# Kernel optimization log

Hardware: AMD Instinct MI355X
Metric: run time of the kernel (lower is better)

The kernel has to match this reference:

```python
import jax, jax.numpy as jnp
import numpy as np

D_SUMMARY = 128
N_LAYERS = 24
N_HEADS = 16
D_HEAD = 64
HIDDEN = 512
ACTIVE_MIN = 12
ROT = 16
THETA = 10000.0
B, P = 16, 128
L_ACT = N_LAYERS - ACTIVE_MIN
OUT_DIM = N_HEADS * 2 * D_HEAD


def setup_inputs() -> dict:
    key = jax.random.key(0)
    k1, k2, k3, k4, k5, k6 = jax.random.split(key, 6)
    summary_stack = jax.random.normal(k1, (B, P, D_SUMMARY), jnp.float32)
    positions = jnp.sort(jax.random.randint(k2, (P,), 0, 8192))
    s1 = 1.0 / np.sqrt(D_SUMMARY)
    s2 = 1.0 / np.sqrt(HIDDEN)
    W1 = jax.random.uniform(k3, (L_ACT, D_SUMMARY, HIDDEN), jnp.float32, -s1, s1)
    b1 = jax.random.uniform(k4, (L_ACT, HIDDEN), jnp.float32, -s1, s1)
    W2 = jax.random.uniform(k5, (L_ACT, HIDDEN, OUT_DIM), jnp.float32, -s2, s2)
    b2 = jax.random.uniform(k6, (L_ACT, OUT_DIM), jnp.float32, -s2, s2)
    return {"summary_stack": summary_stack, "positions": positions,
            "W1": W1, "b1": b1, "W2": W2, "b2": b2}


def reference(summary_stack, positions, W1, b1, W2, b2):
    # Batched 2-layer MLP across all active layers (grouped GEMM)
    h = jax.nn.relu(jnp.einsum('bps,lsh->lbph', summary_stack, W1) + b1[:, None, None, :])
    kv = jnp.einsum('lbph,lho->lbpo', h, W2) + b2[:, None, None, :]
    kv = kv.reshape(L_ACT, B, P, N_HEADS, 2, D_HEAD)
    k = jnp.transpose(kv[..., 0, :], (0, 1, 3, 2, 4))  # (L,B,H,P,D)
    v = jnp.transpose(kv[..., 1, :], (0, 1, 3, 2, 4))
    # RoPE on first ROT dims of K
    inv_freq = 1.0 / (THETA ** (jnp.arange(0, ROT, 2, dtype=jnp.float32) / ROT))
    freqs = positions.astype(jnp.float32)[:, None] * inv_freq[None, :]  # (P, ROT//2)
    emb = jnp.concatenate([freqs, freqs], axis=-1)  # (P, ROT)
    cos, sin = jnp.cos(emb), jnp.sin(emb)
    k_rot, k_pass = k[..., :ROT], k[..., ROT:]
    rot_half = jnp.concatenate([-k_rot[..., ROT // 2:], k_rot[..., :ROT // 2]], axis=-1)
    k_emb = k_rot * cos + rot_half * sin
    k = jnp.concatenate([k_emb, k_pass], axis=-1)
    # Inactive layers get zero K/V
    zeros = jnp.zeros((ACTIVE_MIN, B, N_HEADS, P, D_HEAD), k.dtype)
    k_all = jnp.concatenate([zeros, k], axis=0)
    v_all = jnp.concatenate([zeros, v], axis=0)
    return jnp.stack([k_all, v_all], axis=1)  # (n_layers, 2, B, H, P, D)
```

## Files before the change

### kernel.cpp

```cpp
#include <hip/hip_runtime.h>
#include <hip/hip_bf16.h>

#define L_ACT   12
#define BDIM    16
#define PDIM    128
#define DSUM    128
#define HID     512
#define ODIM    2048
#define NHEAD   16
#define DHEAD   64
#define MROWS   2048

typedef short s16x4  __attribute__((ext_vector_type(4)));
typedef short short8 __attribute__((ext_vector_type(8)));
typedef float f32x4  __attribute__((ext_vector_type(4)));

__device__ __forceinline__ void gload_lds16(const __hip_bfloat16* g, __hip_bfloat16* l) {
  __builtin_amdgcn_global_load_lds(
      (const __attribute__((address_space(1))) unsigned int*)g,
      (__attribute__((address_space(3))) unsigned int*)l, 16, 0, 0);
}

__device__ __forceinline__ short f2bf(float x) {
  __hip_bfloat16 h = __float2bfloat16(x);
  return *reinterpret_cast<short*>(&h);
}

__global__ __launch_bounds__(256) void zerofill_kernel(f32x4* __restrict__ p, int n16) {
  int stride = gridDim.x * 256;
  for (int i = blockIdx.x * 256 + threadIdx.x; i < n16; i += stride)
    p[i] = {0.f, 0.f, 0.f, 0.f};
}

__global__ __launch_bounds__(256) void gemm1_128(
    const float* __restrict__ summary,
    const float* __restrict__ W1,
    const int*   __restrict__ positions,
    const float* __restrict__ bias,
    __hip_bfloat16* __restrict__ Hall,
    const float* __restrict__ W2,
    __hip_bfloat16* __restrict__ W2T,
    float* __restrict__ cs,
    f32x4* __restrict__ zeroBase, int doZero) {
  const int KTOT = DSUM, NTOT = HID;
  __shared__ __hip_bfloat16 shbuf[24576];
  __hip_bfloat16* ldsB2 = shbuf;
  __hip_bfloat16* ldsA  = shbuf + 16384;
  const int l    = blockIdx.z;
  const int n0   = blockIdx.x * 128;
  const int m0   = blockIdx.y * 128;
  const int tid  = threadIdx.x;
  const int wid  = tid >> 6;
  const int lane = tid & 63;
  const int wr = wid >> 1, wc = wid & 1;
  const int bid = blockIdx.x + 4 * blockIdx.y + 64 * blockIdx.z;

  if (bid == 0) {
#pragma unroll
    for (int q = 0; q < 4; ++q) {
      int i = q * 256 + tid;
      int p = i >> 3, f = i & 7;
      double inv = pow(10000.0, -(double)f / 8.0);
      double ang = (double)positions[p] * inv;
      cs[i]        = (float)cos(ang);
      cs[1024 + i] = (float)sin(ang);
    }
  }

  {
    const float* Wp = W1 + (size_t)l * DSUM * HID + n0;
#pragma unroll
    for (int q = 0; q < 16; ++q) {
      int g  = q * 256 + tid;
      int j4 = g >> 7;
      int r  = g & 127;
      s16x4 w;
#pragma unroll
      for (int jj = 0; jj < 4; ++jj)
        w[jj] = f2bf(Wp[(size_t)(j4 * 4 + jj) * HID + r]);
      int chunk = (j4 >> 1) ^ (r & 7);
      *(s16x4*)((char*)ldsB2 + r * 256 + chunk * 16 + (j4 & 1) * 8) = w;
    }
  }

  f32x4 acc[4][4];
#pragma unroll
  for (int m = 0; m < 4; ++m)
#pragma unroll
    for (int n = 0; n < 4; ++n)
      acc[m][n] = {0.f, 0.f, 0.f, 0.f};

  const int kq = lane >> 4;

  for (int kt = 0; kt < KTOT / 64; ++kt) {
    __syncthreads();
#pragma unroll
    for (int j = 0; j < 8; ++j) {
      int s = j * 256 + tid;
      int r = s >> 4, g = s & 15;
      f32x4 v = *(const f32x4*)(summary + (size_t)(m0 + r) * DSUM + kt * 64 + g * 4);
      s16x4 w;
      w[0] = f2bf(v[0]); w[1] = f2bf(v[1]); w[2] = f2bf(v[2]); w[3] = f2bf(v[3]);
      int ch = g >> 1;
      *(s16x4*)((char*)ldsA + r * 128 + ((ch ^ (r & 7)) << 4) + (g & 1) * 8) = w;
    }
    __syncthreads();
#pragma unroll
    for (int kk = 0; kk < 2; ++kk) {
      short8 af[4], bfr[4];
#pragma unroll
      for (int m = 0; m < 4; ++m) {
        int row = wr * 64 + m * 16 + (lane & 15);
        int off = (kk * 64 + kq * 16) ^ ((row & 7) << 4);
        af[m] = *(const short8*)((const char*)ldsA + row * 128 + off);
      }
#pragma unroll
      for (int n = 0; n < 4; ++n) {
        int row = wc * 64 + n * 16 + (lane & 15);
        int chunk = (kt * 8 + kk * 4 + kq) ^ (row & 7);
        bfr[n] = *(const short8*)((const char*)ldsB2 + row * 256 + chunk * 16);
      }
#pragma unroll
      for (int m = 0; m < 4; ++m)
#pragma unroll
        for (int n = 0; n < 4; ++n)
          acc[m][n] = __builtin_amdgcn_mfma_f32_16x16x32_bf16(af[m], bfr[n], acc[m][n], 0, 0, 0);
    }
  }

  __syncthreads();
#pragma unroll
  for (int n = 0; n < 4; ++n) {
    int col = wc * 64 + n * 16 + (lane & 15);
    float bb = bias[l * NTOT + n0 + col];
#pragma unroll
    for (int m = 0; m < 4; ++m) {
      int rowb = wr * 64 + m * 16 + ((lane >> 4) << 2);
#pragma unroll
      for (int j = 0; j < 4; ++j) {
        float v = acc[m][n][j] + bb;
        v = v > 0.f ? v : 0.f;
        shbuf[(rowb + j) * 136 + col] = __float2bfloat16(v);
      }
    }
  }
  __syncthreads();
  {
    __hip_bfloat16* H = Hall + (size_t)l * MROWS * HID;
#pragma unroll
    for (int i = 0; i < 8; ++i) {
      int idx = i * 256 + tid;
      int row = idx >> 4, seg = idx & 15;
      short8 v = *(const short8*)(shbuf + row * 136 + seg * 8);
      *(short8*)(H + (size_t)(m0 + row) * HID + n0 + seg * 8) = v;
    }
  }
  __syncthreads();

  {
    float* tb0 = (float*)shbuf;
    float* tb1 = (float*)shbuf + 1056;
    const int tx = tid & 31, ty = tid >> 5;
    const int tbase = bid * 16;
    const f32x4 z = {0.f, 0.f, 0.f, 0.f};
    f32x4* zp = zeroBase + (size_t)bid * 8192;
    float rvA0, rvA1, rvA2, rvA3, rvB0, rvB1, rvB2, rvB3;

#define W2_LOAD(P, tt_) do {                                                \
      int t_ = tbase + (tt_);                                               \
      int lz_ = t_ >> 10, rem_ = t_ & 1023;                                 \
      int j0_ = (rem_ >> 6) * 32, o0_ = (rem_ & 63) * 32;                   \
      const float* ip_ = W2 + (size_t)lz_ * HID * ODIM                      \
                       + (size_t)(j0_ + ty) * ODIM + o0_ + tx;              \
      P##0 = ip_[0];                                                        \
      P##1 = ip_[(size_t)8 * ODIM];                                         \
      P##2 = ip_[(size_t)16 * ODIM];                                        \
      P##3 = ip_[(size_t)24 * ODIM];                                        \
    } while (0)

#define W2_WRITE(buf, P) do {                                               \
      (buf)[(ty +  0) * 33 + tx] = P##0;                                    \
      (buf)[(ty +  8) * 33 + tx] = P##1;                                    \
      (buf)[(ty + 16) * 33 + tx] = P##2;                                    \
      (buf)[(ty + 24) * 33 + tx] = P##3;                                    \
    } while (0)

#define W2_STORE(buf, tt_) do {                                             \
      int t_ = tbase + (tt_);                                               \
      int lz_ = t_ >> 10, rem_ = t_ & 1023;                                 \
      int j0_ = (rem_ >> 6) * 32, o0_ = (rem_ & 63) * 32;                   \
      __hip_bfloat16* op_ = W2T + (size_t)lz_ * HID * ODIM;                 \
      _Pragma("unroll")                                                     \
      for (int r_ = 0; r_ < 4; ++r_)                                        \
        op_[(size_t)(o0_ + ty + 8 * r_) * HID + j0_ + tx] =                 \
            __float2bfloat16((buf)[tx * 33 + ty + 8 * r_]);                 \
    } while (0)

#define ZCHUNK(tt_) do { if (doZero && (tt_) < 8) {                         \
      _Pragma("unroll")                                                     \
      for (int q_ = 0; q_ < 4; ++q_)                                        \
        __builtin_nontemporal_store(z, zp + ((tt_) * 4 + q_) * 256 + tid);  \
    } } while (0)

    W2_LOAD(rvA, 0);
    W2_LOAD(rvB, 1);
    W2_WRITE(tb0, rvA);
    __syncthreads();
#pragma unroll 1
    for (int tt = 0; tt < 16; tt += 2) {
      if (tt + 2 < 16) W2_LOAD(rvA, tt + 2);
      W2_STORE(tb0, tt);
      W2_WRITE(tb1, rvB);
      ZCHUNK(tt);
      __syncthreads();
      if (tt + 3 < 16) W2_LOAD(rvB, tt + 3);
      W2_STORE(tb1, tt + 1);
      if (tt + 2 < 16) W2_WRITE(tb0, rvA);
      ZCHUNK(tt + 1);
      __syncthreads();
    }
#undef W2_LOAD
#undef W2_WRITE
#undef W2_STORE
#undef ZCHUNK
  }
}

__global__ __launch_bounds__(256, 2) void gemm2_pipe(
    const __hip_bfloat16* __restrict__ Aall,
    const __hip_bfloat16* __restrict__ Ball,
    const float* __restrict__ bias,
    const float* __restrict__ cs,
    float* __restrict__ O,
    f32x4* __restrict__ zeroBase, int doZero) {
  __shared__ __hip_bfloat16 lds[3 * 12288];
  const int orig = blockIdx.x + 16 * blockIdx.y + 128 * blockIdx.z;
  const int nw   = (orig & 7) * 192 + (orig >> 3);
  const int bx   = nw & 15;
  const int by   = (nw >> 4) & 7;
  const int l    = nw >> 7;
  const int n0  = bx * 128;
  const int m0  = by * 256;
  const int tid = threadIdx.x;
  const int wid = tid >> 6, lane = tid & 63;
  const int wm  = wid >> 1, wn = wid & 1;
  const __hip_bfloat16* A  = Aall + (size_t)l * MROWS * HID;
  const __hip_bfloat16* Bt = Ball + (size_t)l * ODIM * HID;
  f32x4* zq = zeroBase + (size_t)nw * 4096;
  const f32x4 zv = {0.f, 0.f, 0.f, 0.f};

  f32x4 acc[8][4];
#pragma unroll
  for (int m = 0; m < 8; ++m)
#pragma unroll
    for (int n = 0; n < 4; ++n)
      acc[m][n] = {0.f, 0.f, 0.f, 0.f};

  int ra[4], ca[4], rb[2], cb[2];
#pragma unroll
  for (int j = 0; j < 4; ++j) {
    int cx = j * 256 + tid;
    ra[j] = cx >> 2; ca[j] = (cx & 3) ^ ((ra[j] >> 1) & 3);
  }
#pragma unroll
  for (int j = 0; j < 2; ++j) {
    int cx = j * 256 + tid;
    rb[j] = cx >> 2; cb[j] = (cx & 3) ^ ((rb[j] >> 1) & 3);
  }

#define STAGE_A(slot, kt) do {                                                      \
    _Pragma("unroll")                                                               \
    for (int j_ = 0; j_ < 4; ++j_)                                                  \
      gload_lds16(A + (size_t)(m0 + ra[j_]) * HID + (kt) * 32 + ca[j_] * 8,         \
                  lds + (slot) * 12288 + j_ * 2048 + wid * 512);                    \
  } while (0)
#define STAGE_B(slot, kt) do {                                                      \
    _Pragma("unroll")                                                               \
    for (int j_ = 0; j_ < 2; ++j_)                                                  \
      gload_lds16(Bt + (size_t)(n0 + rb[j_]) * HID + (kt) * 32 + cb[j_] * 8,        \
                  lds + (slot) * 12288 + 8192 + j_ * 2048 + wid * 512);             \
  } while (0)

  const int kq   = lane >> 4;
  const int rl15 = lane & 15;

#define LD_FRAG(dst, base, rr) do {                                                 \
    int r_ = (rr);                                                                  \
    int off_ = r_ * 64 + ((kq ^ ((r_ >> 1) & 3)) << 4);                             \
    dst = *(const short8*)((const char*)(base) + off_);                             \
  } while (0)

  STAGE_A(0, 0); STAGE_B(0, 0);
  STAGE_A(1, 1); STAGE_B(1, 1);
  asm volatile("s_waitcnt vmcnt(6)" ::: "memory");
  __builtin_amdgcn_s_barrier();

  const int NT = HID / 32;
  for (int t = 0; t < NT; ++t) {
    const int cur = t % 3;
    const __hip_bfloat16* sa = lds + cur * 12288;
    const __hip_bfloat16* sb = sa + 8192;
    short8 af[4], bfr[4];

    if (doZero)
      __builtin_nontemporal_store(zv, zq + t * 256 + tid);

#pragma unroll
    for (int n = 0; n < 4; ++n) LD_FRAG(bfr[n], sb, wn * 64 + n * 16 + rl15);
#pragma unroll
    for (int mi = 0; mi < 4; ++mi) LD_FRAG(af[mi], sa, wm * 128 + mi * 16 + rl15);
    if (t + 2 < NT) STAGE_A((t + 2) % 3, t + 2);
    __builtin_amdgcn_s_barrier();
    __builtin_amdgcn_s_setprio(1);
#pragma unroll
    for (int mi = 0; mi < 4; ++mi)
#pragma unroll
      for (int n = 0; n < 4; ++n)
        acc[mi][n] = __builtin_amdgcn_mfma_f32_16x16x32_bf16(af[mi], bfr[n], acc[mi][n], 0, 0, 0);
    __builtin_amdgcn_s_setprio(0);
    __builtin_amdgcn_s_barrier();

#pragma unroll
    for (int mi = 0; mi < 4; ++mi) LD_FRAG(af[mi], sa, wm * 128 + 64 + mi * 16 + rl15);
    if (t + 2 < NT) STAGE_B((t + 2) % 3, t + 2);
    __builtin_amdgcn_s_barrier();
    __builtin_amdgcn_s_setprio(1);
#pragma unroll
    for (int mi = 0; mi < 4; ++mi)
#pragma unroll
      for (int n = 0; n < 4; ++n)
        acc[4 + mi][n] = __builtin_amdgcn_mfma_f32_16x16x32_bf16(af[mi], bfr[n], acc[4 + mi][n], 0, 0, 0);
    __builtin_amdgcn_s_setprio(0);
    if (t < NT - 2)       asm volatile("s_waitcnt vmcnt(6)" ::: "memory");
    else if (t == NT - 2) asm volatile("s_waitcnt vmcnt(0)" ::: "memory");
    __builtin_amdgcn_s_barrier();
  }
#undef STAGE_A
#undef STAGE_B
#undef LD_FRAG

  __syncthreads();
  const int head = bx;
  const int tkv  = wn;
  const int bidx = by * 2 + wm;
  float* slab = O + ((((size_t)(l + L_ACT) * 2 + tkv) * BDIM + bidx) * NHEAD + head) * (PDIM * DHEAD);
  const bool ropeWave = (tkv == 0);

  float bb[4];
#pragma unroll
  for (int n = 0; n < 4; ++n) bb[n] = bias[l * ODIM + n0 + wn * 64 + n * 16 + rl15];

  float* Tw = (float*)lds + wid * 2080;

#pragma unroll
  for (int c = 0; c < 4; ++c) {
#pragma unroll
    for (int mh = 0; mh < 2; ++mh) {
      int mf = c * 2 + mh;
      int pl = mh * 16 + (lane >> 4) * 4;
#pragma unroll
      for (int n = 0; n < 4; ++n) {
#pragma unroll
        for (int j = 0; j < 4; ++j) {
          float v = acc[mf][n][j] + bb[n];
          if (ropeWave && n == 0) {
            float partner = __shfl_xor(v, 8);
            int p = c * 32 + pl + j;
            float cv = cs[p * 8 + (lane & 7)];
            float sv = cs[1024 + p * 8 + (lane & 7)];
            v = v * cv + (((lane & 15) < 8) ? -partner : partner) * sv;
          }
          Tw[(pl + j) * 65 + n * 16 + rl15] = v;
        }
      }
    }
#pragma unroll
    for (int it = 0; it < 8; ++it) {
      int pl = it * 4 + (lane >> 4);
      f32x4 vv = *(const f32x4*)(Tw + pl * 65 + rl15 * 4);
      __builtin_nontemporal_store(vv, (f32x4*)(slab + (size_t)(c * 32 + pl) * DHEAD + rl15 * 4));
    }
  }
}

extern "C" void kernel_launch(void* const* d_in, const int* in_sizes, int n_in,
                              void* d_out, int out_size, void* d_ws, size_t ws_size,
                              hipStream_t stream) {
  const float* summary   = (const float*)d_in[0];
  const int*   positions = (const int*)d_in[1];
  const float* W1 = (const float*)d_in[2];
  const float* b1 = (const float*)d_in[3];
  const float* W2 = (const float*)d_in[4];
  const float* b2 = (const float*)d_in[5];
  float* out = (float*)d_out;

  const size_t SCRATCH_BYTES = 25165824ULL + 25165824ULL + 8192ULL;
  const bool useWs = (ws_size >= SCRATCH_BYTES);
  char* sc = useWs ? (char*)d_ws : (char*)d_out;
  __hip_bfloat16* h_bf = (__hip_bfloat16*)sc;
  __hip_bfloat16* W2T  = (__hip_bfloat16*)(sc + 25165824);
  float*          cs   = (float*)(sc + 50331648);

  gemm1_128<<<dim3(HID / 128, MROWS / 128, L_ACT), 256, 0, stream>>>(
      summary, W1, positions, b1, h_bf, W2, W2T, cs,
      (f32x4*)((char*)d_out + 100663296), useWs ? 1 : 0);
  gemm2_pipe<<<dim3(ODIM / 128, MROWS / 256, L_ACT), 256, 0, stream>>>(
      h_bf, W2T, b2, cs, out, (f32x4*)d_out, useWs ? 1 : 0);

  if (!useWs)
    zerofill_kernel<<<2048, 256, 0, stream>>>((f32x4*)d_out, 12582912);
}
```

Measured before the change: 124.4 us.

## Overlap W2 prefetch and zero-fill stores with GEMM1 using LDS-only barriers

Issues the first W2 tile loads before the GEMM1 main loop and spreads the zero-fill stores for inactive layers across the GEMM1 k-loop and epilogue, so global memory traffic overlaps with MFMA work. It also swaps __syncthreads for a barrier that waits only on LDS counters (lgkmcnt), so in-flight global loads and stores do not stall each barrier. This keeps the prefetched registers live across the GEMM, which raises register pressure. It also relies on global stores never needing ordering at these barriers.

```diff
diff --git a/kernel.cpp b/kernel.cpp
--- a/kernel.cpp
+++ b/kernel.cpp
@@ -25,6 +25,11 @@
   __hip_bfloat16 h = __float2bfloat16(x);
   return *reinterpret_cast<short*>(&h);
 }
+
+#define LBAR() do {                                                   \
+    asm volatile("s_waitcnt lgkmcnt(0)" ::: "memory");                \
+    __builtin_amdgcn_s_barrier();                                     \
+  } while (0)
 
 __global__ __launch_bounds__(256) void zerofill_kernel(f32x4* __restrict__ p, int n16) {
   int stride = gridDim.x * 256;
@@ -55,6 +60,9 @@
   const int wr = wid >> 1, wc = wid & 1;
   const int bid = blockIdx.x + 4 * blockIdx.y + 64 * blockIdx.z;
 
+  const f32x4 z = {0.f, 0.f, 0.f, 0.f};
+  f32x4* zp = zeroBase + (size_t)bid * 8192;
+
   if (bid == 0) {
 #pragma unroll
     for (int q = 0; q < 4; ++q) {
@@ -67,104 +75,9 @@
     }
   }
 
-  {
-    const float* Wp = W1 + (size_t)l * DSUM * HID + n0;
-#pragma unroll
-    for (int q = 0; q < 16; ++q) {
-      int g  = q * 256 + tid;
-      int j4 = g >> 7;
-      int r  = g & 127;
-      s16x4 w;
-#pragma unroll
-      for (int jj = 0; jj < 4; ++jj)
-        w[jj] = f2bf(Wp[(size_t)(j4 * 4 + jj) * HID + r]);
-      int chunk = (j4 >> 1) ^ (r & 7);
-      *(s16x4*)((char*)ldsB2 + r * 256 + chunk * 16 + (j4 & 1) * 8) = w;
-    }
-  }
-
-  f32x4 acc[4][4];
-#pragma unroll
-  for (int m = 0; m < 4; ++m)
-#pragma unroll
-    for (int n = 0; n < 4; ++n)
-      acc[m][n] = {0.f, 0.f, 0.f, 0.f};
-
-  const int kq = lane >> 4;
-
-  for (int kt = 0; kt < KTOT / 64; ++kt) {
-    __syncthreads();
-#pragma unroll
-    for (int j = 0; j < 8; ++j) {
-      int s = j * 256 + tid;
-      int r = s >> 4, g = s & 15;
-      f32x4 v = *(const f32x4*)(summary + (size_t)(m0 + r) * DSUM + kt * 64 + g * 4);
-      s16x4 w;
-      w[0] = f2bf(v[0]); w[1] = f2bf(v[1]); w[2] = f2bf(v[2]); w[3] = f2bf(v[3]);
-      int ch = g >> 1;
-      *(s16x4*)((char*)ldsA + r * 128 + ((ch ^ (r & 7)) << 4) + (g & 1) * 8) = w;
-    }
-    __syncthreads();
-#pragma unroll
-    for (int kk = 0; kk < 2; ++kk) {
-      short8 af[4], bfr[4];
-#pragma unroll
-      for (int m = 0; m < 4; ++m) {
-        int row = wr * 64 + m * 16 + (lane & 15);
-        int off = (kk * 64 + kq * 16) ^ ((row & 7) << 4);
-        af[m] = *(const short8*)((const char*)ldsA + row * 128 + off);
-      }
-#pragma unroll
-      for (int n = 0; n < 4; ++n) {
-        int row = wc * 64 + n * 16 + (lane & 15);
-        int chunk = (kt * 8 + kk * 4 + kq) ^ (row & 7);
-        bfr[n] = *(const short8*)((const char*)ldsB2 + row * 256 + chunk * 16);
-      }
-#pragma unroll
-      for (int m = 0; m < 4; ++m)
-#pragma unroll
-        for (int n = 0; n < 4; ++n)
-          acc[m][n] = __builtin_amdgcn_mfma_f32_16x16x32_bf16(af[m], bfr[n], acc[m][n], 0, 0, 0);
-    }
-  }
-
-  __syncthreads();
-#pragma unroll
-  for (int n = 0; n < 4; ++n) {
-    int col = wc * 64 + n * 16 + (lane & 15);
-    float bb = bias[l * NTOT + n0 + col];
-#pragma unroll
-    for (int m = 0; m < 4; ++m) {
-      int rowb = wr * 64 + m * 16 + ((lane >> 4) << 2);
-#pragma unroll
-      for (int j = 0; j < 4; ++j) {
-        float v = acc[m][n][j] + bb;
-        v = v > 0.f ? v : 0.f;
-        shbuf[(rowb + j) * 136 + col] = __float2bfloat16(v);
-      }
-    }
-  }
-  __syncthreads();
-  {
-    __hip_bfloat16* H = Hall + (size_t)l * MROWS * HID;
-#pragma unroll
-    for (int i = 0; i < 8; ++i) {
-      int idx = i * 256 + tid;
-      int row = idx >> 4, seg = idx & 15;
-      short8 v = *(const short8*)(shbuf + row * 136 + seg * 8);
-      *(short8*)(H + (size_t)(m0 + row) * HID + n0 + seg * 8) = v;
-    }
-  }
-  __syncthreads();
-
-  {
-    float* tb0 = (float*)shbuf;
-    float* tb1 = (float*)shbuf + 1056;
-    const int tx = tid & 31, ty = tid >> 5;
-    const int tbase = bid * 16;
-    const f32x4 z = {0.f, 0.f, 0.f, 0.f};
-    f32x4* zp = zeroBase + (size_t)bid * 8192;
-    float rvA0, rvA1, rvA2, rvA3, rvB0, rvB1, rvB2, rvB3;
+  const int tx = tid & 31, ty = tid >> 5;
+  const int tbase = bid * 16;
+  float rvA0, rvA1, rvA2, rvA3, rvB0, rvB1, rvB2, rvB3;
 
 #define W2_LOAD(P, tt_) do {                                                \
       int t_ = tbase + (tt_);                                               \
@@ -178,6 +91,113 @@
       P##3 = ip_[(size_t)24 * ODIM];                                        \
     } while (0)
 
+  {
+    const float* Wp = W1 + (size_t)l * DSUM * HID + n0;
+#pragma unroll
+    for (int q = 0; q < 16; ++q) {
+      int g  = q * 256 + tid;
+      int j4 = g >> 7;
+      int r  = g & 127;
+      s16x4 w;
+#pragma unroll
+      for (int jj = 0; jj < 4; ++jj)
+        w[jj] = f2bf(Wp[(size_t)(j4 * 4 + jj) * HID + r]);
+      int chunk = (j4 >> 1) ^ (r & 7);
+      *(s16x4*)((char*)ldsB2 + r * 256 + chunk * 16 + (j4 & 1) * 8) = w;
+    }
+  }
+
+  W2_LOAD(rvA, 0);
+  W2_LOAD(rvB, 1);
+
+  f32x4 acc[4][4];
+#pragma unroll
+  for (int m = 0; m < 4; ++m)
+#pragma unroll
+    for (int n = 0; n < 4; ++n)
+      acc[m][n] = {0.f, 0.f, 0.f, 0.f};
+
+  const int kq = lane >> 4;
+
+  for (int kt = 0; kt < KTOT / 64; ++kt) {
+    LBAR();
+    if (doZero) {
+#pragma unroll
+      for (int q = 0; q < 4; ++q)
+        __builtin_nontemporal_store(z, zp + (kt * 4 + q) * 256 + tid);
+    }
+#pragma unroll
+    for (int j = 0; j < 8; ++j) {
+      int s = j * 256 + tid;
+      int r = s >> 4, g = s & 15;
+      f32x4 v = *(const f32x4*)(summary + (size_t)(m0 + r) * DSUM + kt * 64 + g * 4);
+      s16x4 w;
+      w[0] = f2bf(v[0]); w[1] = f2bf(v[1]); w[2] = f2bf(v[2]); w[3] = f2bf(v[3]);
+      int ch = g >> 1;
+      *(s16x4*)((char*)ldsA + r * 128 + ((ch ^ (r & 7)) << 4) + (g & 1) * 8) = w;
+    }
+    LBAR();
+#pragma unroll
+    for (int kk = 0; kk < 2; ++kk) {
+      short8 af[4], bfr[4];
+#pragma unroll
+      for (int m = 0; m < 4; ++m) {
+        int row = wr * 64 + m * 16 + (lane & 15);
+        int off = (kk * 64 + kq * 16) ^ ((row & 7) << 4);
+        af[m] = *(const short8*)((const char*)ldsA + row * 128 + off);
+      }
+#pragma unroll
+      for (int n = 0; n < 4; ++n) {
+        int row = wc * 64 + n * 16 + (lane & 15);
+        int chunk = (kt * 8 + kk * 4 + kq) ^ (row & 7);
+        bfr[n] = *(const short8*)((const char*)ldsB2 + row * 256 + chunk * 16);
+      }
+#pragma unroll
+      for (int m = 0; m < 4; ++m)
+#pragma unroll
+        for (int n = 0; n < 4; ++n)
+          acc[m][n] = __builtin_amdgcn_mfma_f32_16x16x32_bf16(af[m], bfr[n], acc[m][n], 0, 0, 0);
+    }
+  }
+
+  LBAR();
+#pragma unroll
+  for (int n = 0; n < 4; ++n) {
+    int col = wc * 64 + n * 16 + (lane & 15);
+    float bb = bias[l * NTOT + n0 + col];
+#pragma unroll
+    for (int m = 0; m < 4; ++m) {
+      int rowb = wr * 64 + m * 16 + ((lane >> 4) << 2);
+#pragma unroll
+      for (int j = 0; j < 4; ++j) {
+        float v = acc[m][n][j] + bb;
+        v = v > 0.f ? v : 0.f;
+        shbuf[(rowb + j) * 136 + col] = __float2bfloat16(v);
+      }
+    }
+  }
+  if (doZero) {
+#pragma unroll
+    for (int i = 0; i < 8; ++i)
+      __builtin_nontemporal_store(z, zp + (8 + i) * 256 + tid);
+  }
+  LBAR();
+  {
+    __hip_bfloat16* H = Hall + (size_t)l * MROWS * HID;
+#pragma unroll
+    for (int i = 0; i < 8; ++i) {
+      int idx = i * 256 + tid;
+      int row = idx >> 4, seg = idx & 15;
+      short8 v = *(const short8*)(shbuf + row * 136 + seg * 8);
+      *(short8*)(H + (size_t)(m0 + row) * HID + n0 + seg * 8) = v;
+    }
+  }
+  LBAR();
+
+  {
+    float* tb0 = (float*)shbuf;
+    float* tb1 = (float*)shbuf + 1056;
+
 #define W2_WRITE(buf, P) do {                                               \
       (buf)[(ty +  0) * 33 + tx] = P##0;                                    \
       (buf)[(ty +  8) * 33 + tx] = P##1;                                    \
@@ -196,28 +216,26 @@
             __float2bfloat16((buf)[tx * 33 + ty + 8 * r_]);                 \
     } while (0)
 
-#define ZCHUNK(tt_) do { if (doZero && (tt_) < 8) {                         \
+#define ZCHUNK(tt_) do { if (doZero && (tt_) < 4) {                         \
       _Pragma("unroll")                                                     \
       for (int q_ = 0; q_ < 4; ++q_)                                        \
-        __builtin_nontemporal_store(z, zp + ((tt_) * 4 + q_) * 256 + tid);  \
+        __builtin_nontemporal_store(z, zp + (16 + (tt_) * 4 + q_) * 256 + tid); \
     } } while (0)
 
-    W2_LOAD(rvA, 0);
-    W2_LOAD(rvB, 1);
     W2_WRITE(tb0, rvA);
-    __syncthreads();
+    LBAR();
 #pragma unroll 1
     for (int tt = 0; tt < 16; tt += 2) {
       if (tt + 2 < 16) W2_LOAD(rvA, tt + 2);
       W2_STORE(tb0, tt);
       W2_WRITE(tb1, rvB);
       ZCHUNK(tt);
-      __syncthreads();
+      LBAR();
       if (tt + 3 < 16) W2_LOAD(rvB, tt + 3);
       W2_STORE(tb1, tt + 1);
       if (tt + 2 < 16) W2_WRITE(tb0, rvA);
       ZCHUNK(tt + 1);
-      __syncthreads();
+      LBAR();
     }
 #undef W2_LOAD
 #undef W2_WRITE
```

Result: faster. 121.4 us (-2.4%).
